# Kernel tuning notes

Hardware: AMD Instinct MI355X
Metric: run time of the kernel (lower is better)

Reference implementation:

```python
import jax, jax.numpy as jnp
import numpy as np

EPS = 1e-12

def disk_map(n_bins):
    # Precompute the disk rasterization index map (static, numpy).
    w = 2 * n_bins + 1
    ii, jj = np.meshgrid(np.arange(w), np.arange(w), indexing='ij')
    inside = (ii - n_bins) ** 2 + (jj - n_bins) ** 2 <= (n_bins + 0.25) ** 2
    flat = (w * ii + jj)[inside]
    dmap = np.zeros(w * w, dtype=np.int32)
    dmap[flat] = np.arange(flat.size, dtype=np.int32)
    return jnp.asarray(dmap), int(flat.size)

def soft_abs(re, im):
    return jnp.sqrt(re * re + im * im + EPS)

def setup_inputs():
    key = jax.random.key(0)
    k1, k2, k3, k4 = jax.random.split(key, 4)
    N, E, C = 50000, 1600000, 8
    x = jax.random.normal(k1, (N, C, 2), jnp.float32)          # complex as (re, im)
    supp_edges = jax.random.randint(k2, (E, 2), 0, N)           # (j, i): source -> target
    ln = jax.random.normal(k3, (E, 2), jnp.float32)             # log map, complex
    wxp = jax.random.normal(k4, (E, 2), jnp.float32)            # transport * weights, complex
    return {"x": x, "supp_edges": supp_edges, "ln": ln, "wxp": wxp, "n_bins": 2}

def reference(x, supp_edges, ln, wxp, n_bins):
    n_bins = int(n_bins)
    w = 2 * n_bins + 1
    dMap, dS = disk_map(n_bins)
    N, C = x.shape[0], x.shape[1]

    xC = jax.lax.complex(x[..., 0], x[..., 1])      # (N, C)
    lnC = jax.lax.complex(ln[..., 0], ln[..., 1])   # (E,)
    wC = jax.lax.complex(wxp[..., 0], wxp[..., 1])  # (E,)

    src = supp_edges[:, 0]
    tgt = supp_edges[:, 1]

    x_src = xC[src]                                  # (E, C) gather
    # softAngle -> unit phase; aligned = ln * conj(exp(i*angle(x_src)))
    ang = jnp.arctan2(x_src.imag, x_src.real)
    unit_conj = jax.lax.complex(jnp.cos(ang), -jnp.sin(ang))
    aligned = lnC[:, None] * unit_conj               # (E, C)

    # rasterize: bilinear weights + disk-bin indices
    p = aligned * n_bins
    pr, pi = p.real, p.imag                          # (E, C) each
    nb = jnp.float32(n_bins)
    pCx = jnp.clip(jnp.ceil(pr), -nb, nb)
    pCy = jnp.clip(jnp.ceil(pi), -nb, nb)
    pFx = jnp.clip(jnp.floor(pr), -nb, nb)
    pFy = jnp.clip(jnp.floor(pi), -nb, nb)

    r0 = (pCx - pr) * (pCy - pi)
    r1 = (pr - pFx) * (pi - pFy)
    r2 = (pr - pFx) * (pCy - pi)
    r3 = (pCx - pr) * (pi - pFy)
    rast = jnp.stack([r0, r1, r2, r3], axis=-1)      # (E, C, 4)

    pCxi, pCyi = pCx.astype(jnp.int32), pCy.astype(jnp.int32)
    pFxi, pFyi = pFx.astype(jnp.int32), pFy.astype(jnp.int32)
    i0 = dMap[w * (pFxi + n_bins) + (pFyi + n_bins)]
    i1 = dMap[w * (pCxi + n_bins) + (pCyi + n_bins)]
    i2 = dMap[w * (pCxi + n_bins) + (pFyi + n_bins)]
    i3 = dMap[w * (pFxi + n_bins) + (pCyi + n_bins)]
    ind = jnp.stack([i0, i1, i2, i3], axis=-1)       # (E, C, 4)

    # origin mask (equivalent to the torch nonzero filter; x==0 -> zero contribution)
    nz = ((x_src.real != 0) | (x_src.imag != 0)).astype(jnp.float32)
    xW = x_src * wC[:, None] * nz                    # (E, C)

    target = (C * dS) * tgt[:, None, None] + dS * jnp.arange(C, dtype=tgt.dtype)[None, :, None]
    flat_idx = (target + ind).reshape(-1)            # (E*C*4,)
    vals = (xW[:, :, None] * rast).reshape(-1)       # (E*C*4,) complex

    hist = jnp.zeros(N * C * dS, dtype=xC.dtype).at[flat_idx].add(vals)
    hist = hist.reshape(N, C, dS)
    return soft_abs(hist.real, hist.imag)
```

## Files before the change

kernel.cpp:

```cpp
#include <hip/hip_runtime.h>
#include <math.h>

constexpr int NB  = 2;
constexpr int DS  = 21;
constexpr int C   = 8;
constexpr int CAP = 96;

__device__ __forceinline__ bool near_boundary(float v) {
    return fabsf(v) < 2.0002f && fabsf(v - rintf(v)) < 3e-5f;
}

__global__ __launch_bounds__(256) void pack_kernel(
        const int2* __restrict__ edges,
        int*        __restrict__ cursors,
        int2*       __restrict__ slots, int E) {
    int stride = gridDim.x * blockDim.x;
    for (int e = blockIdx.x * blockDim.x + threadIdx.x; e < E; e += stride) {
        int2 ed = edges[e];
        int pos = atomicAdd(&cursors[ed.y], 1);
        if (pos < CAP) slots[(size_t)ed.y * CAP + pos] = make_int2(ed.x, e);
    }
}

__global__ __launch_bounds__(256) void accum_kernel(
        const float2* __restrict__ x,
        const float2* __restrict__ ln,
        const float2* __restrict__ wxp,
        const int*    __restrict__ cursors,
        const int2*   __restrict__ slots,
        float*        __restrict__ out, int N) {
    const int lane = threadIdx.x & 63;
    const int c    = lane & 7;
    const int el   = lane >> 3;
    const int nwaves  = (gridDim.x * blockDim.x) >> 6;
    const int wid     = (blockIdx.x * blockDim.x + threadIdx.x) >> 6;
    const int ngroups = (N + 7) >> 3;

    for (int g = wid; g < ngroups; g += nwaves) {
        const int  t  = g * 8 + el;
        const bool tv = (t < N);
        int cnt = tv ? cursors[t] : 0;
        cnt = (cnt > CAP) ? CAP : cnt;
        const size_t base = (size_t)t * CAP;

        float aRe[25], aIm[25];
        #pragma unroll
        for (int i = 0; i < 25; ++i) { aRe[i] = 0.0f; aIm[i] = 0.0f; }

        int2 slA, slB; float2 xA, lvA, wvA;
        if (cnt > 0) {
            slA = slots[base];
            slB = (cnt > 1) ? slots[base + 1] : slA;
            xA  = x[slA.x * C + c];
            lvA = ln[slA.y];
            wvA = wxp[slA.y];
        }

        for (int e = 0; e < cnt; ++e) {
            float2 xs = xA, lv = lvA, wv = wvA;
            if (e + 1 < cnt) {
                xA  = x[slB.x * C + c];
                lvA = ln[slB.y];
                wvA = wxp[slB.y];
                if (e + 2 < cnt) slB = slots[base + e + 2];
            }

            float rr = xs.x * xs.x + xs.y * xs.y;
            float uc, us;
            if (rr > 0.0f) {
                float inv = 1.0f / sqrtf(rr);
                uc = xs.x * inv; us = xs.y * inv;
            } else { uc = 1.0f; us = 0.0f; }

            float pr = 2.0f * (lv.x * uc + lv.y * us);
            float pi = 2.0f * (lv.y * uc - lv.x * us);

            if ((near_boundary(pr) || near_boundary(pi)) && rr > 0.0f) {
                double dang = atan2((double)xs.y, (double)xs.x);
                float ang = (float)dang;
                float uc2 = (float)cos((double)ang);
                float us2 = (float)sin((double)ang);
                float ar = __fadd_rn(__fmul_rn(lv.x, uc2), __fmul_rn(lv.y, us2));
                float ai = __fsub_rn(__fmul_rn(lv.y, uc2), __fmul_rn(lv.x, us2));
                pr = __fmul_rn(2.0f, ar);
                pi = __fmul_rn(2.0f, ai);
            }

            const float nb = 2.0f;
            float pCx = fminf(fmaxf(ceilf(pr),  -nb), nb);
            float pCy = fminf(fmaxf(ceilf(pi),  -nb), nb);
            float pFx = fminf(fmaxf(floorf(pr), -nb), nb);
            float pFy = fminf(fmaxf(floorf(pi), -nb), nb);

            float zx = (pCx != pFx) ? 1.0f : 0.0f;
            float zy = (pCy != pFy) ? 1.0f : 0.0f;
            float nzm = (xs.x != 0.0f || xs.y != 0.0f) ? 1.0f : 0.0f;
            float m = zx * zy * nzm;

            float xwr = (xs.x * wv.x - xs.y * wv.y) * m;
            float xwi = (xs.x * wv.y + xs.y * wv.x) * m;

            float wx[5], wy[5];
            #pragma unroll
            for (int a = 0; a < 5; ++a) {
                wx[a] = fmaxf(0.0f, 1.0f - fabsf(pr - (float)(a - 2)));
                wy[a] = fmaxf(0.0f, 1.0f - fabsf(pi - (float)(a - 2)));
            }

            #pragma unroll
            for (int a = 0; a < 5; ++a) {
                float tr = xwr * wx[a], ti = xwi * wx[a];
                #pragma unroll
                for (int y = 0; y < 5; ++y) {
                    aRe[a * 5 + y] = fmaf(tr, wy[y], aRe[a * 5 + y]);
                    aIm[a * 5 + y] = fmaf(ti, wy[y], aIm[a * 5 + y]);
                }
            }
        }

        if (tv) {
            float* outp = out + (size_t)t * (C * DS) + c * DS;
            float b0r = aRe[1] + aRe[0] + aRe[4] + aRe[20] + aRe[24];
            float b0i = aIm[1] + aIm[0] + aIm[4] + aIm[20] + aIm[24];
            outp[0] = sqrtf(b0r * b0r + b0i * b0i + 1e-12f);
            const int cells[20] = { 2, 3,
                                    5, 6, 7, 8, 9,
                                   10,11,12,13,14,
                                   15,16,17,18,19,
                                   21,22,23 };
            #pragma unroll
            for (int b = 0; b < 20; ++b) {
                float re = aRe[cells[b]], im = aIm[cells[b]];
                outp[b + 1] = sqrtf(re * re + im * im + 1e-12f);
            }
        }
    }
}

extern "C" void kernel_launch(void* const* d_in, const int* in_sizes, int n_in,
                              void* d_out, int out_size, void* d_ws, size_t ws_size,
                              hipStream_t stream) {
    const float2* x     = (const float2*)d_in[0];
    const int2*   edges = (const int2*)d_in[1];
    const float2* ln    = (const float2*)d_in[2];
    const float2* wxp   = (const float2*)d_in[3];

    const int E = in_sizes[1] / 2;
    const int N = in_sizes[0] / (C * 2);

    char* ws = (char*)d_ws;
    int*  cursors = (int*)(ws + 0);
    int2* slots   = (int2*)(ws + (1 << 20));

    hipMemsetAsync(cursors, 0, (size_t)N * sizeof(int), stream);

    pack_kernel<<<2048, 256, 0, stream>>>(edges, cursors, slots, E);

    const int ngroups = (N + 7) / 8;
    const int nblocks = (ngroups + 3) / 4;
    accum_kernel<<<nblocks, 256, 0, stream>>>(x, ln, wxp, cursors, slots,
                                              (float*)d_out, N);
}
```

Baseline: 305.4 us.

## Shard edge binning per XCD and merge, storing only edge ids

Replaces the single global bucket pass with per-XCD sharded cursors and buckets, so atomics stay local to each XCD's L2, then merges the shards into a compact per-target slot list. Slots now hold only the edge id, and the accumulate kernel re-reads the source index from the edge array through an extra dependent load in the prefetch chain. This adds a merge kernel, a larger memset, and per-shard capacity limits (24 per shard, 72 total) that could drop edges on skewed inputs.

```diff
diff --git a/kernel.cpp b/kernel.cpp
--- a/kernel.cpp
+++ b/kernel.cpp
@@ -1,33 +1,63 @@
 #include <hip/hip_runtime.h>
 #include <math.h>
 
-constexpr int NB  = 2;
-constexpr int DS  = 21;
-constexpr int C   = 8;
-constexpr int CAP = 96;
+constexpr int NB   = 2;
+constexpr int DS   = 21;
+constexpr int C    = 8;
+constexpr int NXCD = 8;
+constexpr int CAP8 = 24;
+constexpr int CAPF = 72;
 
 __device__ __forceinline__ bool near_boundary(float v) {
     return fabsf(v) < 2.0002f && fabsf(v - rintf(v)) < 3e-5f;
 }
 
-__global__ __launch_bounds__(256) void pack_kernel(
-        const int2* __restrict__ edges,
-        int*        __restrict__ cursors,
-        int2*       __restrict__ slots, int E) {
+__global__ __launch_bounds__(256) void shard_pack(
+        const int4* __restrict__ e2,
+        int*        __restrict__ cur8,
+        int*        __restrict__ shard,
+        int E2, int N) {
+    const int xcd = blockIdx.x & (NXCD - 1);
+    int* mycur = cur8 + (size_t)xcd * N;
+    int* mysh  = shard + (size_t)xcd * N * CAP8;
     int stride = gridDim.x * blockDim.x;
-    for (int e = blockIdx.x * blockDim.x + threadIdx.x; e < E; e += stride) {
-        int2 ed = edges[e];
-        int pos = atomicAdd(&cursors[ed.y], 1);
-        if (pos < CAP) slots[(size_t)ed.y * CAP + pos] = make_int2(ed.x, e);
+    for (int i = blockIdx.x * blockDim.x + threadIdx.x; i < E2; i += stride) {
+        int4 v = e2[i];
+        int p0 = atomicAdd(&mycur[v.y], 1);
+        if (p0 < CAP8) mysh[v.y * CAP8 + p0] = 2 * i;
+        int p1 = atomicAdd(&mycur[v.w], 1);
+        if (p1 < CAP8) mysh[v.w * CAP8 + p1] = 2 * i + 1;
     }
+}
+
+__global__ __launch_bounds__(256) void merge_kernel(
+        const int* __restrict__ cur8,
+        const int* __restrict__ shard,
+        int*       __restrict__ slots,
+        int*       __restrict__ counts, int N) {
+    int t = blockIdx.x * blockDim.x + threadIdx.x;
+    if (t >= N) return;
+    int total = 0;
+    int* dst = slots + (size_t)t * CAPF;
+    for (int x = 0; x < NXCD; ++x) {
+        int c8 = cur8[(size_t)x * N + t];
+        c8 = (c8 > CAP8) ? CAP8 : c8;
+        const int* sp = shard + ((size_t)x * N + t) * CAP8;
+        for (int k = 0; k < c8; ++k) {
+            if (total < CAPF) dst[total] = sp[k];
+            ++total;
+        }
+    }
+    counts[t] = (total > CAPF) ? CAPF : total;
 }
 
 __global__ __launch_bounds__(256) void accum_kernel(
         const float2* __restrict__ x,
+        const int2*   __restrict__ edges,
         const float2* __restrict__ ln,
         const float2* __restrict__ wxp,
-        const int*    __restrict__ cursors,
-        const int2*   __restrict__ slots,
+        const int*    __restrict__ counts,
+        const int*    __restrict__ slots,
         float*        __restrict__ out, int N) {
     const int lane = threadIdx.x & 63;
     const int c    = lane & 7;
@@ -39,30 +69,35 @@
     for (int g = wid; g < ngroups; g += nwaves) {
         const int  t  = g * 8 + el;
         const bool tv = (t < N);
-        int cnt = tv ? cursors[t] : 0;
-        cnt = (cnt > CAP) ? CAP : cnt;
-        const size_t base = (size_t)t * CAP;
+        int cnt = tv ? counts[t] : 0;
+        const size_t sbase = (size_t)t * CAPF;
 
         float aRe[25], aIm[25];
         #pragma unroll
         for (int i = 0; i < 25; ++i) { aRe[i] = 0.0f; aIm[i] = 0.0f; }
 
-        int2 slA, slB; float2 xA, lvA, wvA;
+        int eidB = 0, srcB = 0, slotC = 0;
+        float2 xA, lvA, wvA;
         if (cnt > 0) {
-            slA = slots[base];
-            slB = (cnt > 1) ? slots[base + 1] : slA;
-            xA  = x[slA.x * C + c];
-            lvA = ln[slA.y];
-            wvA = wxp[slA.y];
+            int eid0 = slots[sbase];
+            int src0 = edges[eid0].x;
+            xA  = x[src0 * C + c];
+            lvA = ln[eid0];
+            wvA = wxp[eid0];
+            if (cnt > 1) { eidB = slots[sbase + 1]; srcB = edges[eidB].x; }
+            if (cnt > 2) { slotC = slots[sbase + 2]; }
         }
 
         for (int e = 0; e < cnt; ++e) {
             float2 xs = xA, lv = lvA, wv = wvA;
             if (e + 1 < cnt) {
-                xA  = x[slB.x * C + c];
-                lvA = ln[slB.y];
-                wvA = wxp[slB.y];
-                if (e + 2 < cnt) slB = slots[base + e + 2];
+                xA  = x[srcB * C + c];
+                lvA = ln[eidB];
+                wvA = wxp[eidB];
+                if (e + 2 < cnt) {
+                    eidB = slotC; srcB = edges[slotC].x;
+                    if (e + 3 < cnt) slotC = slots[sbase + e + 3];
+                }
             }
 
             float rr = xs.x * xs.x + xs.y * xs.y;
@@ -149,15 +184,20 @@
     const int N = in_sizes[0] / (C * 2);
 
     char* ws = (char*)d_ws;
-    int*  cursors = (int*)(ws + 0);
-    int2* slots   = (int2*)(ws + (1 << 20));
-
-    hipMemsetAsync(cursors, 0, (size_t)N * sizeof(int), stream);
-
-    pack_kernel<<<2048, 256, 0, stream>>>(edges, cursors, slots, E);
+    int* cur8   = (int*)(ws + 0);
+    int* counts = (int*)(ws + (2  << 20));
+    int* slots  = (int*)(ws + (4  << 20));
+    int* shard  = (int*)(ws + (20 << 20));
+
+    hipMemsetAsync(cur8, 0, (size_t)NXCD * N * sizeof(int), stream);
+
+    shard_pack<<<2048, 256, 0, stream>>>((const int4*)edges, cur8, shard,
+                                         E / 2, N);
+    merge_kernel<<<(N + 255) / 256, 256, 0, stream>>>(cur8, shard, slots,
+                                                      counts, N);
 
     const int ngroups = (N + 7) / 8;
     const int nblocks = (ngroups + 3) / 4;
-    accum_kernel<<<nblocks, 256, 0, stream>>>(x, ln, wxp, cursors, slots,
+    accum_kernel<<<nblocks, 256, 0, stream>>>(x, edges, ln, wxp, counts, slots,
                                               (float*)d_out, N);
 }
```

Result: slower. 367.2 us (+20.2%).
